# Kernel optimization log

Measured on AMD Instinct MI355X. Metric: run time of the kernel, lower is better.

Reference implementation:

```python
import jax, jax.numpy as jnp
import numpy as np

B, L, H, W, C = 2, 32, 16, 16, 32  # L must equal channels for the view() to be consistent
CH = L  # conv channel count


def setup_inputs() -> dict:
    key = jax.random.key(0)
    k1, k2, k3, k4, k5 = jax.random.split(key, 5)
    return {
        "inputs": jax.random.normal(k1, (B, L, H, W, C), dtype=jnp.float32),
        "W1": jax.random.normal(k2, (CH // 2, CH), dtype=jnp.float32) * 0.1,
        "b1": jax.random.normal(k3, (CH // 2,), dtype=jnp.float32) * 0.1,
        "W2": jax.random.normal(k4, (CH, CH), dtype=jnp.float32) * 0.1,
        "b2": jax.random.normal(k5, (CH,), dtype=jnp.float32) * 0.1,
        "gamma": jnp.ones((1,), dtype=jnp.float32),
    }


def reference(inputs, W1, b1, W2, b2, gamma):
    b, l, h, w, c = inputs.shape
    n = l * h * w  # flattened 'spatial' positions after the (buggy-but-faithful) reshape
    # conv1x1 over dim-1 (torch Conv3d treats dim-1 as channels)
    x1 = jnp.einsum('ol,blhwc->bohwc', W1, inputs) + b1[None, :, None, None, None]
    # permute (0,4,1,2,3) then view(b, c//2, l*h*w)
    x1 = jnp.transpose(x1, (0, 4, 1, 2, 3)).reshape(b, c // 2, n)
    # attn[b, i, j] = sum_k x1[b, k, i] * x1[b, k, j]; softmax over last dim
    attn = jax.nn.softmax(jnp.einsum('bki,bkj->bij', x1, x1), axis=-1)  # [b, n, n]
    x2 = jnp.einsum('ol,blhwc->bohwc', W2, inputs) + b2[None, :, None, None, None]
    x2 = jnp.transpose(x2, (0, 4, 1, 2, 3)).reshape(b, c, n)
    # x2 @ attn^T : out[b, c, i] = sum_j x2[b, c, j] * attn[b, i, j]
    out = jnp.einsum('bcj,bij->bci', x2, attn)
    out = jnp.transpose(out.reshape(b, c, l, h, w), (0, 2, 3, 4, 1))
    return out * gamma + inputs
```

## Files before the change

### kernel.cpp

```cpp
#include <hip/hip_runtime.h>
#include <hip/hip_bf16.h>
#include <math.h>

typedef __bf16 bf16x8 __attribute__((ext_vector_type(8)));
typedef __bf16 bf16x2 __attribute__((ext_vector_type(2)));
typedef float  floatx16 __attribute__((ext_vector_type(16)));
typedef unsigned u32x4 __attribute__((ext_vector_type(4)));

#define KQ_ELEMS (2 * 8192 * 16)
#define OPART_OFF 1572864
#define SQRT_LOG2E 1.2011224087864498f
#define LSPLIT 3

__global__ __launch_bounds__(512) void proj_kernel(
    const float* __restrict__ in, const float* __restrict__ W1,
    const float* __restrict__ b1, const float* __restrict__ W2,
    const float* __restrict__ b2,
    __hip_bfloat16* __restrict__ Kq, __hip_bfloat16* __restrict__ Vswz)
{
    __shared__ float Xs[32][32];
    __shared__ float W1s[16 * 32];
    __shared__ float W2s[32 * 32];
    const int t = threadIdx.x;
    const int bid = blockIdx.x;
    const int b = bid >> 8;
    const int hw = bid & 255;

    {
        int l = t >> 4, cs = (t & 15) * 2;
        float2 v = *(const float2*)(in + (((size_t)b * 32 + l) * 256 + hw) * 32 + cs);
        *(float2*)&Xs[l][cs] = v;
    }
    if (t < 128) *(float4*)&W1s[t * 4] = *(const float4*)(W1 + t * 4);
    if (t < 256) *(float4*)&W2s[t * 4] = *(const float4*)(W2 + t * 4);
    __syncthreads();

    const int c = t & 31;
    const int g = t >> 5;

    {
        int o = g;
        float a0 = b1[o], a1 = 0.f;
#pragma unroll
        for (int l = 0; l < 16; ++l) {
            a0 += W1s[o * 32 + l] * Xs[l][c];
            a1 += W1s[o * 32 + 16 + l] * Xs[16 + l][c];
        }
        float acc = a0 + a1;
        int k = c >> 1;
        int i = (c & 1) * 4096 + o * 256 + hw;
        Kq[((size_t)b * 8192 + i) * 16 + k] = __float2bfloat16(acc * SQRT_LOG2E);
    }
#pragma unroll
    for (int oo = 0; oo < 2; ++oo) {
        int o = g * 2 + oo;
        float a0 = b2[o], a1 = 0.f;
#pragma unroll
        for (int l = 0; l < 16; ++l) {
            a0 += W2s[o * 32 + l] * Xs[l][c];
            a1 += W2s[o * 32 + 16 + l] * Xs[16 + l][c];
        }
        float acc = a0 + a1;
        int jt = o * 8 + (hw >> 5);
        int f  = (hw >> 4) & 1;
        int hh = (hw >> 2) & 1;
        int idx = (hw & 3) | (((hw >> 3) & 1) << 2);
        Vswz[(size_t)b * 262144 + jt * 1024 + f * 512 + hh * 256 + c * 8 + idx] =
            __float2bfloat16(acc);
    }
}

__global__ __launch_bounds__(256, 4) void flash_kernel(
    const __hip_bfloat16* __restrict__ Kq, const __hip_bfloat16* __restrict__ Vswz,
    __hip_bfloat16* __restrict__ Opart, float* __restrict__ Lpart)
{
    const int t = threadIdx.x;
    const int lane = t & 63;
    const int wv = t >> 6;
    const int m = lane & 31;
    const int h = lane >> 5;

    const int bid = blockIdx.x;
    const int s = bid & ((1 << LSPLIT) - 1);
    const int itile = (bid >> LSPLIT) & 63;
    const int b = bid >> (LSPLIT + 6);
    const int i0 = itile * 128 + wv * 32;
    const int niter = (8192 >> LSPLIT) >> 5;
    const int jt0 = s * niter;

    const __hip_bfloat16* Kb = Kq + (size_t)b * 8192 * 16;
    const __hip_bfloat16* Vb = Vswz + (size_t)b * 262144 + h * 256 + m * 8;

    const bf16x8 bq = *(const bf16x8*)(Kb + (size_t)(i0 + m) * 16 + h * 8);

    floatx16 oa = {};
    float l0 = 0.f, l1 = 0.f, l2 = 0.f, l3 = 0.f;

    bf16x8 ak = *(const bf16x8*)(Kb + (size_t)(jt0 * 32 + m) * 16 + h * 8);
    bf16x8 vb0 = *(const bf16x8*)(Vb + (size_t)jt0 * 1024 + 0);
    bf16x8 vb1 = *(const bf16x8*)(Vb + (size_t)jt0 * 1024 + 512);

#pragma unroll 2
    for (int it = 0; it < niter; ++it) {
        const bf16x8 cak = ak;
        const bf16x8 cv0 = vb0, cv1 = vb1;
        if (it + 1 < niter) {
            const int jn = jt0 + it + 1;
            ak  = *(const bf16x8*)(Kb + (size_t)(jn * 32 + m) * 16 + h * 8);
            vb0 = *(const bf16x8*)(Vb + (size_t)jn * 1024 + 0);
            vb1 = *(const bf16x8*)(Vb + (size_t)jn * 1024 + 512);
        }

        floatx16 sc = __builtin_amdgcn_mfma_f32_32x32x16_bf16(cak, bq, (floatx16){}, 0, 0, 0);

#pragma unroll
        for (int half = 0; half < 2; ++half) {
            u32x4 pau;
#pragma unroll
            for (int gg = 0; gg < 2; ++gg) {
                const int g = half * 2 + gg;
                float e0 = __builtin_amdgcn_exp2f(sc[4 * g + 0]);
                float e1 = __builtin_amdgcn_exp2f(sc[4 * g + 1]);
                float e2 = __builtin_amdgcn_exp2f(sc[4 * g + 2]);
                float e3 = __builtin_amdgcn_exp2f(sc[4 * g + 3]);
                l0 += e0; l1 += e1; l2 += e2; l3 += e3;
#if defined(__has_builtin) && __has_builtin(__builtin_amdgcn_cvt_pk_bf16_f32)
                bf16x2 pk0 = __builtin_amdgcn_cvt_pk_bf16_f32(e0, e1);
                bf16x2 pk1 = __builtin_amdgcn_cvt_pk_bf16_f32(e2, e3);
#else
                bf16x2 pk0 = {(__bf16)e0, (__bf16)e1};
                bf16x2 pk1 = {(__bf16)e2, (__bf16)e3};
#endif
                pau[gg * 2 + 0] = __builtin_bit_cast(unsigned, pk0);
                pau[gg * 2 + 1] = __builtin_bit_cast(unsigned, pk1);
            }
            bf16x8 pa = __builtin_bit_cast(bf16x8, pau);
            oa = __builtin_amdgcn_mfma_f32_32x32x16_bf16(pa, half ? cv1 : cv0, oa, 0, 0, 0);
        }
    }

    float l = (l0 + l1) + (l2 + l3);
    l += __shfl_xor(l, 32);
    const float rinv = __builtin_amdgcn_rcpf(l);

#pragma unroll
    for (int r = 0; r < 16; ++r) {
        int iloc = (r & 3) + 8 * (r >> 2) + 4 * h;
        float lr = __shfl(rinv, iloc);
        size_t row = (size_t)b * 8192 + i0 + iloc;
        Opart[((row << LSPLIT) | s) * 32 + m] = __float2bfloat16(oa[r] * lr);
    }
    if (h == 0)
        Lpart[(((size_t)b * 8192 + i0 + m) << LSPLIT) | s] = l;
}

__global__ __launch_bounds__(256) void combine_kernel(
    const unsigned short* __restrict__ Opart, const float* __restrict__ Lpart,
    const float* __restrict__ in, const float* __restrict__ gamma,
    float* __restrict__ out)
{
    const int gid = blockIdx.x * 256 + threadIdx.x;
    const int row = gid >> 4;
    const int c2 = (gid & 15) * 2;
    const unsigned short* op = Opart + (((size_t)row << LSPLIT)) * 32 + c2;
    const float* lp = Lpart + ((size_t)row << LSPLIT);
    float4 l0 = *(const float4*)(lp);
    float4 l1 = *(const float4*)(lp + 4);
    float ls8[8] = {l0.x, l0.y, l0.z, l0.w, l1.x, l1.y, l1.z, l1.w};
    float ax = 0.f, ay = 0.f;
    float lsum = 0.f;
#pragma unroll
    for (int s = 0; s < (1 << LSPLIT); ++s) {
        ushort2 u = *(const ushort2*)(op + s * 32);
        float ls = ls8[s];
        ax += ls * __uint_as_float((unsigned)u.x << 16);
        ay += ls * __uint_as_float((unsigned)u.y << 16);
        lsum += ls;
    }
    const size_t base = (size_t)row * 32 + c2;
    float2 x = *(const float2*)(in + base);
    const float gl = gamma[0] / lsum;
    float2 r;
    r.x = ax * gl + x.x;
    r.y = ay * gl + x.y;
    *(float2*)(out + base) = r;
}

extern "C" void kernel_launch(void* const* d_in, const int* in_sizes, int n_in,
                              void* d_out, int out_size, void* d_ws, size_t ws_size,
                              hipStream_t stream) {
    const float* in = (const float*)d_in[0];
    const float* W1 = (const float*)d_in[1];
    const float* b1 = (const float*)d_in[2];
    const float* W2 = (const float*)d_in[3];
    const float* b2 = (const float*)d_in[4];
    const float* gamma = (const float*)d_in[5];
    float* out = (float*)d_out;

    __hip_bfloat16* Kq = (__hip_bfloat16*)d_ws;
    __hip_bfloat16* Vswz = Kq + KQ_ELEMS;
    __hip_bfloat16* Opart = (__hip_bfloat16*)((char*)d_ws + OPART_OFF);
    float* Lpart = (float*)(Opart + ((size_t)16384 << LSPLIT) * 32);

    proj_kernel<<<512, 512, 0, stream>>>(in, W1, b1, W2, b2, Kq, Vswz);
    flash_kernel<<<2 * 64 * (1 << LSPLIT), 256, 0, stream>>>(Kq, Vswz, Opart, Lpart);
    combine_kernel<<<1024, 256, 0, stream>>>((const unsigned short*)Opart, Lpart, in, gamma, out);
}
```

Baseline: 95.33 us.

## Process two query tiles per wave and double the KV split count

Each wave now handles 64 query rows (two 32-row MFMA tiles) so every loaded K/V fragment feeds two score and two PV MFMAs, halving K/V load traffic per unit of compute. To keep the block count constant, the key dimension split goes from 8 to 16, which doubles the partial output and logsumexp data the combine kernel must read and merge. Register pressure rises from the second accumulator set, and the loop unroll is reduced to 1 to contain it.

```diff
diff --git a/kernel.cpp b/kernel.cpp
--- a/kernel.cpp
+++ b/kernel.cpp
@@ -10,7 +10,7 @@
 #define KQ_ELEMS (2 * 8192 * 16)
 #define OPART_OFF 1572864
 #define SQRT_LOG2E 1.2011224087864498f
-#define LSPLIT 3
+#define LSPLIT 4
 
 __global__ __launch_bounds__(512) void proj_kernel(
     const float* __restrict__ in, const float* __restrict__ W1,
@@ -82,25 +82,27 @@
 
     const int bid = blockIdx.x;
     const int s = bid & ((1 << LSPLIT) - 1);
-    const int itile = (bid >> LSPLIT) & 63;
-    const int b = bid >> (LSPLIT + 6);
-    const int i0 = itile * 128 + wv * 32;
+    const int itile = (bid >> LSPLIT) & 31;
+    const int b = bid >> (LSPLIT + 5);
+    const int i0 = itile * 256 + wv * 64;
     const int niter = (8192 >> LSPLIT) >> 5;
     const int jt0 = s * niter;
 
     const __hip_bfloat16* Kb = Kq + (size_t)b * 8192 * 16;
     const __hip_bfloat16* Vb = Vswz + (size_t)b * 262144 + h * 256 + m * 8;
 
-    const bf16x8 bq = *(const bf16x8*)(Kb + (size_t)(i0 + m) * 16 + h * 8);
-
-    floatx16 oa = {};
-    float l0 = 0.f, l1 = 0.f, l2 = 0.f, l3 = 0.f;
+    const bf16x8 bq0 = *(const bf16x8*)(Kb + (size_t)(i0 + m) * 16 + h * 8);
+    const bf16x8 bq1 = *(const bf16x8*)(Kb + (size_t)(i0 + 32 + m) * 16 + h * 8);
+
+    floatx16 oa0 = {}, oa1 = {};
+    float lA0 = 0.f, lA1 = 0.f, lA2 = 0.f, lA3 = 0.f;
+    float lB0 = 0.f, lB1 = 0.f, lB2 = 0.f, lB3 = 0.f;
 
     bf16x8 ak = *(const bf16x8*)(Kb + (size_t)(jt0 * 32 + m) * 16 + h * 8);
     bf16x8 vb0 = *(const bf16x8*)(Vb + (size_t)jt0 * 1024 + 0);
     bf16x8 vb1 = *(const bf16x8*)(Vb + (size_t)jt0 * 1024 + 512);
 
-#pragma unroll 2
+#pragma unroll 1
     for (int it = 0; it < niter; ++it) {
         const bf16x8 cak = ak;
         const bf16x8 cv0 = vb0, cv1 = vb1;
@@ -111,47 +113,74 @@
             vb1 = *(const bf16x8*)(Vb + (size_t)jn * 1024 + 512);
         }
 
-        floatx16 sc = __builtin_amdgcn_mfma_f32_32x32x16_bf16(cak, bq, (floatx16){}, 0, 0, 0);
+        floatx16 sc0 = __builtin_amdgcn_mfma_f32_32x32x16_bf16(cak, bq0, (floatx16){}, 0, 0, 0);
+        floatx16 sc1 = __builtin_amdgcn_mfma_f32_32x32x16_bf16(cak, bq1, (floatx16){}, 0, 0, 0);
 
 #pragma unroll
         for (int half = 0; half < 2; ++half) {
-            u32x4 pau;
+            u32x4 pau0, pau1;
 #pragma unroll
             for (int gg = 0; gg < 2; ++gg) {
                 const int g = half * 2 + gg;
-                float e0 = __builtin_amdgcn_exp2f(sc[4 * g + 0]);
-                float e1 = __builtin_amdgcn_exp2f(sc[4 * g + 1]);
-                float e2 = __builtin_amdgcn_exp2f(sc[4 * g + 2]);
-                float e3 = __builtin_amdgcn_exp2f(sc[4 * g + 3]);
-                l0 += e0; l1 += e1; l2 += e2; l3 += e3;
+                {
+                    float e0 = __builtin_amdgcn_exp2f(sc0[4 * g + 0]);
+                    float e1 = __builtin_amdgcn_exp2f(sc0[4 * g + 1]);
+                    float e2 = __builtin_amdgcn_exp2f(sc0[4 * g + 2]);
+                    float e3 = __builtin_amdgcn_exp2f(sc0[4 * g + 3]);
+                    lA0 += e0; lA1 += e1; lA2 += e2; lA3 += e3;
 #if defined(__has_builtin) && __has_builtin(__builtin_amdgcn_cvt_pk_bf16_f32)
-                bf16x2 pk0 = __builtin_amdgcn_cvt_pk_bf16_f32(e0, e1);
-                bf16x2 pk1 = __builtin_amdgcn_cvt_pk_bf16_f32(e2, e3);
+                    bf16x2 pk0 = __builtin_amdgcn_cvt_pk_bf16_f32(e0, e1);
+                    bf16x2 pk1 = __builtin_amdgcn_cvt_pk_bf16_f32(e2, e3);
 #else
-                bf16x2 pk0 = {(__bf16)e0, (__bf16)e1};
-                bf16x2 pk1 = {(__bf16)e2, (__bf16)e3};
+                    bf16x2 pk0 = {(__bf16)e0, (__bf16)e1};
+                    bf16x2 pk1 = {(__bf16)e2, (__bf16)e3};
 #endif
-                pau[gg * 2 + 0] = __builtin_bit_cast(unsigned, pk0);
-                pau[gg * 2 + 1] = __builtin_bit_cast(unsigned, pk1);
+                    pau0[gg * 2 + 0] = __builtin_bit_cast(unsigned, pk0);
+                    pau0[gg * 2 + 1] = __builtin_bit_cast(unsigned, pk1);
+                }
+                {
+                    float e0 = __builtin_amdgcn_exp2f(sc1[4 * g + 0]);
+                    float e1 = __builtin_amdgcn_exp2f(sc1[4 * g + 1]);
+                    float e2 = __builtin_amdgcn_exp2f(sc1[4 * g + 2]);
+                    float e3 = __builtin_amdgcn_exp2f(sc1[4 * g + 3]);
+                    lB0 += e0; lB1 += e1; lB2 += e2; lB3 += e3;
+#if defined(__has_builtin) && __has_builtin(__builtin_amdgcn_cvt_pk_bf16_f32)
+                    bf16x2 pk0 = __builtin_amdgcn_cvt_pk_bf16_f32(e0, e1);
+                    bf16x2 pk1 = __builtin_amdgcn_cvt_pk_bf16_f32(e2, e3);
+#else
+                    bf16x2 pk0 = {(__bf16)e0, (__bf16)e1};
+                    bf16x2 pk1 = {(__bf16)e2, (__bf16)e3};
+#endif
+                    pau1[gg * 2 + 0] = __builtin_bit_cast(unsigned, pk0);
+                    pau1[gg * 2 + 1] = __builtin_bit_cast(unsigned, pk1);
+                }
             }
-            bf16x8 pa = __builtin_bit_cast(bf16x8, pau);
-            oa = __builtin_amdgcn_mfma_f32_32x32x16_bf16(pa, half ? cv1 : cv0, oa, 0, 0, 0);
-        }
-    }
-
-    float l = (l0 + l1) + (l2 + l3);
-    l += __shfl_xor(l, 32);
-    const float rinv = __builtin_amdgcn_rcpf(l);
+            const bf16x8 cv = half ? cv1 : cv0;
+            oa0 = __builtin_amdgcn_mfma_f32_32x32x16_bf16(__builtin_bit_cast(bf16x8, pau0), cv, oa0, 0, 0, 0);
+            oa1 = __builtin_amdgcn_mfma_f32_32x32x16_bf16(__builtin_bit_cast(bf16x8, pau1), cv, oa1, 0, 0, 0);
+        }
+    }
+
+    float la = (lA0 + lA1) + (lA2 + lA3);
+    la += __shfl_xor(la, 32);
+    float lb = (lB0 + lB1) + (lB2 + lB3);
+    lb += __shfl_xor(lb, 32);
+    const float rA = __builtin_amdgcn_rcpf(la);
+    const float rB = __builtin_amdgcn_rcpf(lb);
 
 #pragma unroll
     for (int r = 0; r < 16; ++r) {
         int iloc = (r & 3) + 8 * (r >> 2) + 4 * h;
-        float lr = __shfl(rinv, iloc);
-        size_t row = (size_t)b * 8192 + i0 + iloc;
-        Opart[((row << LSPLIT) | s) * 32 + m] = __float2bfloat16(oa[r] * lr);
-    }
-    if (h == 0)
-        Lpart[(((size_t)b * 8192 + i0 + m) << LSPLIT) | s] = l;
+        float lrA = __shfl(rA, iloc);
+        float lrB = __shfl(rB, iloc);
+        size_t rowA = (size_t)b * 8192 + i0 + iloc;
+        Opart[((rowA << LSPLIT) | s) * 32 + m] = __float2bfloat16(oa0[r] * lrA);
+        Opart[(((rowA + 32) << LSPLIT) | s) * 32 + m] = __float2bfloat16(oa1[r] * lrB);
+    }
+    if (h == 0) {
+        Lpart[(((size_t)b * 8192 + i0 + m) << LSPLIT) | s] = la;
+        Lpart[(((size_t)b * 8192 + i0 + 32 + m) << LSPLIT) | s] = lb;
+    }
 }
 
 __global__ __launch_bounds__(256) void combine_kernel(
@@ -164,18 +193,22 @@
     const int c2 = (gid & 15) * 2;
     const unsigned short* op = Opart + (((size_t)row << LSPLIT)) * 32 + c2;
     const float* lp = Lpart + ((size_t)row << LSPLIT);
-    float4 l0 = *(const float4*)(lp);
-    float4 l1 = *(const float4*)(lp + 4);
-    float ls8[8] = {l0.x, l0.y, l0.z, l0.w, l1.x, l1.y, l1.z, l1.w};
+    float ls[1 << LSPLIT];
+#pragma unroll
+    for (int q = 0; q < (1 << LSPLIT) / 4; ++q) {
+        float4 lv = *(const float4*)(lp + q * 4);
+        ls[q * 4 + 0] = lv.x; ls[q * 4 + 1] = lv.y;
+        ls[q * 4 + 2] = lv.z; ls[q * 4 + 3] = lv.w;
+    }
     float ax = 0.f, ay = 0.f;
     float lsum = 0.f;
 #pragma unroll
     for (int s = 0; s < (1 << LSPLIT); ++s) {
         ushort2 u = *(const ushort2*)(op + s * 32);
-        float ls = ls8[s];
-        ax += ls * __uint_as_float((unsigned)u.x << 16);
-        ay += ls * __uint_as_float((unsigned)u.y << 16);
-        lsum += ls;
+        float l = ls[s];
+        ax += l * __uint_as_float((unsigned)u.x << 16);
+        ay += l * __uint_as_float((unsigned)u.y << 16);
+        lsum += l;
     }
     const size_t base = (size_t)row * 32 + c2;
     float2 x = *(const float2*)(in + base);
@@ -203,6 +236,6 @@
     float* Lpart = (float*)(Opart + ((size_t)16384 << LSPLIT) * 32);
 
     proj_kernel<<<512, 512, 0, stream>>>(in, W1, b1, W2, b2, Kq, Vswz);
-    flash_kernel<<<2 * 64 * (1 << LSPLIT), 256, 0, stream>>>(Kq, Vswz, Opart, Lpart);
+    flash_kernel<<<2 * 32 * (1 << LSPLIT), 256, 0, stream>>>(Kq, Vswz, Opart, Lpart);
     combine_kernel<<<1024, 256, 0, stream>>>((const unsigned short*)Opart, Lpart, in, gamma, out);
 }
```

After: 99.29 us. 1.04x slower.
